# Kernel optimization log

Measured on AMD Instinct MI355X. Metric: run time of the kernel, lower is better.

The kernel has to match this reference:

```python
import jax, jax.numpy as jnp
import numpy as np

EMBED_DIM = 1024
NUM_HEADS = 16
HEAD_DIM = EMBED_DIM // NUM_HEADS  # 64


def setup_inputs() -> dict:
    key = jax.random.key(0)
    ks = jax.random.split(key, 9)
    B, S, E, D = 4, 2048, EMBED_DIM, HEAD_DIM
    s_e = 1.0 / np.sqrt(E)
    return {
        "x": jax.random.normal(ks[0], (B, S, E), dtype=jnp.float32),
        "Wq": jax.random.uniform(ks[1], (E, E), jnp.float32, -s_e, s_e),
        "bq": jax.random.uniform(ks[2], (E,), jnp.float32, -s_e, s_e),
        "Wk": jax.random.uniform(ks[3], (E, D), jnp.float32, -s_e, s_e),
        "bk": jax.random.uniform(ks[4], (D,), jnp.float32, -s_e, s_e),
        "Wv": jax.random.uniform(ks[5], (E, D), jnp.float32, -s_e, s_e),
        "bv": jax.random.uniform(ks[6], (D,), jnp.float32, -s_e, s_e),
        "Wo": jax.random.uniform(ks[7], (E, E), jnp.float32, -s_e, s_e),
        "bo": jax.random.uniform(ks[8], (E,), jnp.float32, -s_e, s_e),
    }


def reference(x, Wq, bq, Wk, bk, Wv, bv, Wo, bo):
    B, S, E = x.shape
    H, D = NUM_HEADS, HEAD_DIM
    q = (x @ Wq + bq).reshape(B, S, H, D)           # [B,S,H,D]
    k = x @ Wk + bk                                  # [B,S,D] shared single K head
    v = x @ Wv + bv                                  # [B,S,D] shared single V head
    scale = 1.0 / jnp.sqrt(jnp.asarray(D, x.dtype))
    # broadcast shared K across query heads: [B,H,Sq,Sk]
    scores = jnp.einsum("bqhd,bkd->bhqk", q, k) * scale
    probs = jax.nn.softmax(scores, axis=-1)
    out = jnp.einsum("bhqk,bkd->bqhd", probs, v).reshape(B, S, E)
    return out @ Wo + bo
```

## Files before the change

kernel.cpp:

```cpp
#include <hip/hip_runtime.h>

typedef short  bf16x8 __attribute__((ext_vector_type(8)));
typedef float  f32x4  __attribute__((ext_vector_type(4)));
typedef float  f32x16 __attribute__((ext_vector_type(16)));
typedef unsigned int u32;

__device__ __forceinline__ ushort f2b(float f) {
    union { float f; unsigned u; } c; c.f = f;
    unsigned r = c.u + 0x7fffu + ((c.u >> 16) & 1u);
    return (ushort)(r >> 16);
}

__device__ __forceinline__ unsigned cvtpk(float lo, float hi) {
    unsigned r;
    asm("v_cvt_pk_bf16_f32 %0, %1, %2" : "=v"(r) : "v"(lo), "v"(hi));
    return r;
}

__device__ __forceinline__ float fexp2(float x) {
#if __has_builtin(__builtin_amdgcn_exp2f)
    return __builtin_amdgcn_exp2f(x);
#else
    float r; asm("v_exp_f32 %0, %1" : "=v"(r) : "v"(x)); return r;
#endif
}

__device__ __forceinline__ void gload_lds16(const void* g, void* l) {
    __builtin_amdgcn_global_load_lds(
        (const __attribute__((address_space(1))) u32*)g,
        (__attribute__((address_space(3))) u32*)l, 16, 0, 0);
}

__global__ __launch_bounds__(256) void cast_f32_bf16(const float* __restrict__ in,
                                                     ushort* __restrict__ out, int n) {
    for (int i = (blockIdx.x * blockDim.x + threadIdx.x) * 4; i < n;
         i += gridDim.x * blockDim.x * 4) {
        float4 v = *(const float4*)(in + i);
        ushort4 o;
        o.x = f2b(v.x); o.y = f2b(v.y); o.z = f2b(v.z); o.w = f2b(v.w);
        *(ushort4*)(out + i) = o;
    }
}

__global__ __launch_bounds__(256) void transpose_cast(const float* __restrict__ in,
                                                      ushort* __restrict__ out, int R, int C) {
    __shared__ float tile[32][33];
    int c0 = blockIdx.x * 32, r0 = blockIdx.y * 32;
    int tx = threadIdx.x, ty = threadIdx.y;
#pragma unroll
    for (int i = 0; i < 32; i += 8)
        tile[ty + i][tx] = in[(size_t)(r0 + ty + i) * C + c0 + tx];
    __syncthreads();
#pragma unroll
    for (int i = 0; i < 32; i += 8)
        out[(size_t)(c0 + ty + i) * R + r0 + tx] = f2b(tile[tx][ty + i]);
}

__global__ void concat_bias(const float* __restrict__ bk, const float* __restrict__ bv,
                            float* __restrict__ o) {
    int i = threadIdx.x;
    if (i < 128) o[i] = (i < 64) ? bk[i] : bv[i - 64];
}

__global__ __launch_bounds__(256) void repack_kv(const ushort* __restrict__ kvb,
                                                 ushort* __restrict__ Kc,
                                                 ushort* __restrict__ Vc) {
    __shared__ ushort vl[64][72];
    int t = blockIdx.x, b = blockIdx.y;
    int tid = threadIdx.x;
#pragma unroll
    for (int u = tid; u < 512; u += 256) {
        int s = u >> 3, c = u & 7;
        const ushort* src = kvb + (size_t)(b * 2048 + t * 64 + s) * 128 + c * 8;
        *(uint4*)(Kc + ((size_t)(b * 8 + c) * 2048 + t * 64 + s) * 8) = *(const uint4*)src;
        *(uint4*)(&vl[s][c * 8]) = *(const uint4*)(src + 64);
    }
    __syncthreads();
#pragma unroll
    for (int u = tid; u < 512; u += 256) {
        int sc = u >> 6, d = u & 63;
        ushort tmp[8];
#pragma unroll
        for (int si = 0; si < 8; si++) tmp[si] = vl[sc * 8 + si][d];
        *(uint4*)(Vc + ((size_t)((b * 32 + t) * 8 + sc) * 64 + d) * 8) = *(uint4*)tmp;
    }
}

template <bool OUT_BF16>
__global__ __launch_bounds__(256) void gemm_bt(const ushort* __restrict__ A,
                                               const ushort* __restrict__ BT,
                                               const float* __restrict__ bias,
                                               void* __restrict__ Y, int M, int N, int K,
                                               float scale) {
    __shared__ ushort As[128 * 64];
    __shared__ ushort Bs[128 * 64];

    int nwg = gridDim.x * gridDim.y;
    int bid = blockIdx.y * gridDim.x + blockIdx.x;
    int swz = (bid & 7) * (nwg >> 3) + (bid >> 3);
    int bx = swz % gridDim.x, by = swz / gridDim.x;

    int m0 = by * 128, n0 = bx * 128;
    int t = threadIdx.x;
    int lane = t & 63, wid = t >> 6;
    int wr = wid >> 1, wc = wid & 1;
    int fr = lane & 15, fg = lane >> 4;

    int srow = wid * 32 + (lane >> 3);
    int scol = (lane & 7) * 8;
    const ushort* asrc = A + (size_t)(m0 + srow) * K + scol;
    const ushort* bsrc = BT + (size_t)(n0 + srow) * K + scol;

    f32x4 acc[4][4] = {};

    for (int kb = 0; kb < K; kb += 64) {
#pragma unroll
        for (int op = 0; op < 4; op++) {
            gload_lds16(asrc + kb + (size_t)op * 8 * K, &As[(wid * 32 + op * 8) * 64]);
            gload_lds16(bsrc + kb + (size_t)op * 8 * K, &Bs[(wid * 32 + op * 8) * 64]);
        }
        __syncthreads();
#pragma unroll
        for (int kk = 0; kk < 2; kk++) {
            bf16x8 af[4], bfr[4];
#pragma unroll
            for (int m = 0; m < 4; m++)
                af[m] = *(const bf16x8*)&As[(wr * 64 + m * 16 + fr) * 64 + kk * 32 + fg * 8];
#pragma unroll
            for (int n = 0; n < 4; n++)
                bfr[n] = *(const bf16x8*)&Bs[(wc * 64 + n * 16 + fr) * 64 + kk * 32 + fg * 8];
#pragma unroll
            for (int m = 0; m < 4; m++)
#pragma unroll
                for (int n = 0; n < 4; n++)
                    acc[m][n] = __builtin_amdgcn_mfma_f32_16x16x32_bf16(
                        af[m], bfr[n], acc[m][n], 0, 0, 0);
        }
        __syncthreads();
    }

#pragma unroll
    for (int m = 0; m < 4; m++)
#pragma unroll
        for (int n = 0; n < 4; n++) {
            int col = n0 + wc * 64 + n * 16 + fr;
            float bv = bias[col];
#pragma unroll
            for (int j = 0; j < 4; j++) {
                int row = m0 + wr * 64 + m * 16 + fg * 4 + j;
                float v = (acc[m][n][j] + bv) * scale;
                if (OUT_BF16)
                    ((ushort*)Y)[(size_t)row * N + col] = f2b(v);
                else
                    ((float*)Y)[(size_t)row * N + col] = v;
            }
        }
}

__global__ __launch_bounds__(256, 4) void attn_kernel(const ushort* __restrict__ qb,
                                                      const ushort* __restrict__ Kc,
                                                      const ushort* __restrict__ Vc,
                                                      ushort* __restrict__ ctx) {
    const int S = 2048, E = 1024;
    __shared__ ushort Kb[2][4096];
    __shared__ ushort Vb[2][4096];

    int b = blockIdx.z, h = blockIdx.y;
    int wid = threadIdx.x >> 6, lane = threadIdx.x & 63;
    int q0 = blockIdx.x * 128 + wid * 32;
    int ql = lane & 31, hi = lane >> 5;

    int c0 = wid * 2, c1 = c0 + 1;
    const ushort* ks0 = Kc + (size_t)(b * 8 + c0) * 2048 * 8 + lane * 8;
    const ushort* ks1 = Kc + (size_t)(b * 8 + c1) * 2048 * 8 + lane * 8;
    const ushort* vs0 = Vc + (size_t)(b * 32 * 8 + c0) * 64 * 8 + lane * 8;
    const ushort* vs1 = Vc + (size_t)(b * 32 * 8 + c1) * 64 * 8 + lane * 8;

    const ushort* qbase = qb + (size_t)(b * S + q0 + ql) * E + h * 64 + hi * 8;
    bf16x8 qf0 = *(const bf16x8*)(qbase);
    bf16x8 qf1 = *(const bf16x8*)(qbase + 16);
    bf16x8 qf2 = *(const bf16x8*)(qbase + 32);
    bf16x8 qf3 = *(const bf16x8*)(qbase + 48);

    const ushort* kb0 = &Kb[0][hi * 512 + ql * 8];
    const ushort* vb0 = &Vb[0][hi * 512 + ql * 8];

    f32x16 acc0 = {}, acc1 = {};
    f32x16 lv = {};

    gload_lds16(ks0, &Kb[0][c0 * 512]);
    gload_lds16(ks1, &Kb[0][c1 * 512]);
    gload_lds16(vs0, &Vb[0][c0 * 512]);
    gload_lds16(vs1, &Vb[0][c1 * 512]);
    __syncthreads();

    int cur = 0;
    for (int t = 0; t < 32; ++t) {
        if (t < 31) {
            int nb = cur ^ 1;
            ks0 += 512; ks1 += 512; vs0 += 4096; vs1 += 4096;
            gload_lds16(ks0, &Kb[nb][c0 * 512]);
            gload_lds16(ks1, &Kb[nb][c1 * 512]);
            gload_lds16(vs0, &Vb[nb][c0 * 512]);
            gload_lds16(vs1, &Vb[nb][c1 * 512]);
        }
        const ushort* kp = kb0 + cur * 4096;
        const ushort* vp = vb0 + cur * 4096;

        f32x16 pt0 = {}, pt1 = {};
#pragma unroll
        for (int s = 0; s < 4; s++) {
            bf16x8 kf0 = *(const bf16x8*)(kp + s * 1024);
            bf16x8 kf1 = *(const bf16x8*)(kp + s * 1024 + 256);
            bf16x8 qs = (s == 0) ? qf0 : (s == 1) ? qf1 : (s == 2) ? qf2 : qf3;
            pt0 = __builtin_amdgcn_mfma_f32_32x32x16_bf16(kf0, qs, pt0, 0, 0, 0);
            pt1 = __builtin_amdgcn_mfma_f32_32x32x16_bf16(kf1, qs, pt1, 0, 0, 0);
        }

#pragma unroll
        for (int r = 0; r < 16; r++) pt0[r] = fexp2(pt0[r]);
#pragma unroll
        for (int r = 0; r < 16; r++) pt1[r] = fexp2(pt1[r]);

#pragma unroll
        for (int ks = 0; ks < 4; ks++) {
            float p0, p1, p2, p3, p4, p5, p6, p7;
            if (ks == 0)      { p0=pt0[0]; p1=pt0[1]; p2=pt0[2]; p3=pt0[3];
                                p4=pt0[4]; p5=pt0[5]; p6=pt0[6]; p7=pt0[7]; }
            else if (ks == 1) { p0=pt0[8]; p1=pt0[9]; p2=pt0[10]; p3=pt0[11];
                                p4=pt0[12]; p5=pt0[13]; p6=pt0[14]; p7=pt0[15]; }
            else if (ks == 2) { p0=pt1[0]; p1=pt1[1]; p2=pt1[2]; p3=pt1[3];
                                p4=pt1[4]; p5=pt1[5]; p6=pt1[6]; p7=pt1[7]; }
            else              { p0=pt1[8]; p1=pt1[9]; p2=pt1[10]; p3=pt1[11];
                                p4=pt1[12]; p5=pt1[13]; p6=pt1[14]; p7=pt1[15]; }
            unsigned w0 = cvtpk(p0, p1);
            unsigned w2 = cvtpk(p4, p5);
            asm volatile("v_permlane32_swap_b32 %0, %1" : "+v"(w0), "+v"(w2));
            unsigned w1 = cvtpk(p2, p3);
            unsigned w3 = cvtpk(p6, p7);
            asm volatile("v_permlane32_swap_b32 %0, %1" : "+v"(w1), "+v"(w3));
            bf16x8 pa;
            ((unsigned*)&pa)[0] = w0;
            ((unsigned*)&pa)[1] = w1;
            ((unsigned*)&pa)[2] = w2;
            ((unsigned*)&pa)[3] = w3;

            bf16x8 va0 = *(const bf16x8*)(vp + ks * 1024);
            bf16x8 va1 = *(const bf16x8*)(vp + ks * 1024 + 256);
            acc0 = __builtin_amdgcn_mfma_f32_32x32x16_bf16(va0, pa, acc0, 0, 0, 0);
            acc1 = __builtin_amdgcn_mfma_f32_32x32x16_bf16(va1, pa, acc1, 0, 0, 0);
        }

        lv = lv + pt0;
        lv = lv + pt1;

        __syncthreads();
        cur ^= 1;
    }

    float v[16];
#pragma unroll
    for (int r = 0; r < 16; r++) v[r] = lv[r];
#pragma unroll
    for (int st = 8; st; st >>= 1)
#pragma unroll
        for (int r = 0; r < 8; r++)
            if (r < st) v[r] = v[r] + v[r + st];
    float l = v[0] + __shfl_xor(v[0], 32);
    float inv = 1.f / l;

    ushort* obase = ctx + (size_t)(b * S + q0 + ql) * E + h * 64;
#pragma unroll
    for (int g = 0; g < 4; g++) {
        int d = 8 * g + 4 * hi;
        ushort4 o;
        o.x = f2b(acc0[4 * g + 0] * inv);
        o.y = f2b(acc0[4 * g + 1] * inv);
        o.z = f2b(acc0[4 * g + 2] * inv);
        o.w = f2b(acc0[4 * g + 3] * inv);
        *(ushort4*)(obase + d) = o;
    }
#pragma unroll
    for (int g = 0; g < 4; g++) {
        int d = 32 + 8 * g + 4 * hi;
        ushort4 o;
        o.x = f2b(acc1[4 * g + 0] * inv);
        o.y = f2b(acc1[4 * g + 1] * inv);
        o.z = f2b(acc1[4 * g + 2] * inv);
        o.w = f2b(acc1[4 * g + 3] * inv);
        *(ushort4*)(obase + d) = o;
    }
}

extern "C" void kernel_launch(void* const* d_in, const int* in_sizes, int n_in,
                              void* d_out, int out_size, void* d_ws, size_t ws_size,
                              hipStream_t stream) {
    const int B = 4, S = 2048, E = 1024, D = 64;
    const int M = B * S;
    const float QSCALE = 0.18033688011112042f;

    const float* x  = (const float*)d_in[0];
    const float* Wq = (const float*)d_in[1];
    const float* bq = (const float*)d_in[2];
    const float* Wk = (const float*)d_in[3];
    const float* bk = (const float*)d_in[4];
    const float* Wv = (const float*)d_in[5];
    const float* bv = (const float*)d_in[6];
    const float* Wo = (const float*)d_in[7];
    const float* bo = (const float*)d_in[8];
    float* out = (float*)d_out;

    char* w = (char*)d_ws;
    ushort* xb   = (ushort*)w;                 w += (size_t)M * E * 2;
    ushort* qb   = (ushort*)w;                 w += (size_t)M * E * 2;
    ushort* ctx  = (ushort*)w;                 w += (size_t)M * E * 2;
    ushort* WqT  = (ushort*)w;                 w += (size_t)E * E * 2;
    ushort* WoT  = (ushort*)w;                 w += (size_t)E * E * 2;
    ushort* WkvT = (ushort*)w;                 w += (size_t)128 * E * 2;
    ushort* kvb  = (ushort*)w;                 w += (size_t)M * 128 * 2;
    ushort* Kc   = (ushort*)w;                 w += (size_t)B * 8 * S * 8 * 2;
    ushort* Vc   = (ushort*)w;                 w += (size_t)B * 32 * 8 * 64 * 8 * 2;
    float*  bkv  = (float*)w;                  w += 512;

    cast_f32_bf16<<<2048, 256, 0, stream>>>(x, xb, M * E);
    transpose_cast<<<dim3(32, 32), dim3(32, 8), 0, stream>>>(Wq, WqT, E, E);
    transpose_cast<<<dim3(2, 32),  dim3(32, 8), 0, stream>>>(Wk, WkvT, E, D);
    transpose_cast<<<dim3(2, 32),  dim3(32, 8), 0, stream>>>(Wv, WkvT + (size_t)64 * E, E, D);
    transpose_cast<<<dim3(32, 32), dim3(32, 8), 0, stream>>>(Wo, WoT, E, E);
    concat_bias<<<1, 128, 0, stream>>>(bk, bv, bkv);

    gemm_bt<true><<<dim3(E / 128, M / 128), 256, 0, stream>>>(xb, WqT, bq, qb, M, E, E, QSCALE);
    gemm_bt<true><<<dim3(1, M / 128), 256, 0, stream>>>(xb, WkvT, bkv, kvb, M, 128, E, 1.0f);
    repack_kv<<<dim3(32, 4), 256, 0, stream>>>(kvb, Kc, Vc);

    attn_kernel<<<dim3(S / 128, 16, B), 256, 0, stream>>>(qb, Kc, Vc, ctx);

    gemm_bt<false><<<dim3(E / 128, M / 128), 256, 0, stream>>>(ctx, WoT, bo, (void*)out, M, E, E, 1.0f);
}
```

Before: 183.1 us.

## Fuse Q and KV projections into one QKV GEMM and batch transposes

```diff
diff --git a/kernel.cpp b/kernel.cpp
--- a/kernel.cpp
+++ b/kernel.cpp
@@ -42,9 +42,14 @@
     }
 }
 
-__global__ __launch_bounds__(256) void transpose_cast(const float* __restrict__ in,
-                                                      ushort* __restrict__ out, int R, int C) {
+__global__ __launch_bounds__(256) void transpose_cast2(const float* __restrict__ in0,
+                                                       ushort* __restrict__ out0,
+                                                       const float* __restrict__ in1,
+                                                       ushort* __restrict__ out1,
+                                                       int R, int C) {
     __shared__ float tile[32][33];
+    const float* in = blockIdx.z ? in1 : in0;
+    ushort* out = blockIdx.z ? out1 : out0;
     int c0 = blockIdx.x * 32, r0 = blockIdx.y * 32;
     int tx = threadIdx.x, ty = threadIdx.y;
 #pragma unroll
@@ -56,13 +61,13 @@
         out[(size_t)(c0 + ty + i) * R + r0 + tx] = f2b(tile[tx][ty + i]);
 }
 
-__global__ void concat_bias(const float* __restrict__ bk, const float* __restrict__ bv,
-                            float* __restrict__ o) {
-    int i = threadIdx.x;
-    if (i < 128) o[i] = (i < 64) ? bk[i] : bv[i - 64];
-}
-
-__global__ __launch_bounds__(256) void repack_kv(const ushort* __restrict__ kvb,
+__global__ void concat_bias3(const float* __restrict__ bq, const float* __restrict__ bk,
+                             const float* __restrict__ bv, float* __restrict__ o) {
+    for (int i = threadIdx.x; i < 1152; i += 256)
+        o[i] = (i < 1024) ? bq[i] : (i < 1088) ? bk[i - 1024] : bv[i - 1088];
+}
+
+__global__ __launch_bounds__(256) void repack_kv(const ushort* __restrict__ qkv,
                                                  ushort* __restrict__ Kc,
                                                  ushort* __restrict__ Vc) {
     __shared__ ushort vl[64][72];
@@ -71,7 +76,7 @@
 #pragma unroll
     for (int u = tid; u < 512; u += 256) {
         int s = u >> 3, c = u & 7;
-        const ushort* src = kvb + (size_t)(b * 2048 + t * 64 + s) * 128 + c * 8;
+        const ushort* src = qkv + (size_t)(b * 2048 + t * 64 + s) * 1152 + 1024 + c * 8;
         *(uint4*)(Kc + ((size_t)(b * 8 + c) * 2048 + t * 64 + s) * 8) = *(const uint4*)src;
         *(uint4*)(&vl[s][c * 8]) = *(const uint4*)(src + 64);
     }
@@ -91,7 +96,7 @@
                                                const ushort* __restrict__ BT,
                                                const float* __restrict__ bias,
                                                void* __restrict__ Y, int M, int N, int K,
-                                               float scale) {
+                                               int nq, float scale) {
     __shared__ ushort As[128 * 64];
     __shared__ ushort Bs[128 * 64];
 
@@ -145,10 +150,11 @@
         for (int n = 0; n < 4; n++) {
             int col = n0 + wc * 64 + n * 16 + fr;
             float bv = bias[col];
+            float sc = (col < nq) ? scale : 1.0f;
 #pragma unroll
             for (int j = 0; j < 4; j++) {
                 int row = m0 + wr * 64 + m * 16 + fg * 4 + j;
-                float v = (acc[m][n][j] + bv) * scale;
+                float v = (acc[m][n][j] + bv) * sc;
                 if (OUT_BF16)
                     ((ushort*)Y)[(size_t)row * N + col] = f2b(v);
                 else
@@ -157,11 +163,11 @@
         }
 }
 
-__global__ __launch_bounds__(256, 4) void attn_kernel(const ushort* __restrict__ qb,
+__global__ __launch_bounds__(256, 4) void attn_kernel(const ushort* __restrict__ qkv,
                                                       const ushort* __restrict__ Kc,
                                                       const ushort* __restrict__ Vc,
                                                       ushort* __restrict__ ctx) {
-    const int S = 2048, E = 1024;
+    const int S = 2048, E = 1024, QSTR = 1152;
     __shared__ ushort Kb[2][4096];
     __shared__ ushort Vb[2][4096];
 
@@ -176,7 +182,7 @@
     const ushort* vs0 = Vc + (size_t)(b * 32 * 8 + c0) * 64 * 8 + lane * 8;
     const ushort* vs1 = Vc + (size_t)(b * 32 * 8 + c1) * 64 * 8 + lane * 8;
 
-    const ushort* qbase = qb + (size_t)(b * S + q0 + ql) * E + h * 64 + hi * 8;
+    const ushort* qbase = qkv + (size_t)(b * S + q0 + ql) * QSTR + h * 64 + hi * 8;
     bf16x8 qf0 = *(const bf16x8*)(qbase);
     bf16x8 qf1 = *(const bf16x8*)(qbase + 16);
     bf16x8 qf2 = *(const bf16x8*)(qbase + 32);
@@ -208,6 +214,7 @@
         const ushort* vp = vb0 + cur * 4096;
 
         f32x16 pt0 = {}, pt1 = {};
+        __builtin_amdgcn_s_setprio(1);
 #pragma unroll
         for (int s = 0; s < 4; s++) {
             bf16x8 kf0 = *(const bf16x8*)(kp + s * 1024);
@@ -216,12 +223,14 @@
             pt0 = __builtin_amdgcn_mfma_f32_32x32x16_bf16(kf0, qs, pt0, 0, 0, 0);
             pt1 = __builtin_amdgcn_mfma_f32_32x32x16_bf16(kf1, qs, pt1, 0, 0, 0);
         }
+        __builtin_amdgcn_s_setprio(0);
 
 #pragma unroll
         for (int r = 0; r < 16; r++) pt0[r] = fexp2(pt0[r]);
 #pragma unroll
         for (int r = 0; r < 16; r++) pt1[r] = fexp2(pt1[r]);
 
+        __builtin_amdgcn_s_setprio(1);
 #pragma unroll
         for (int ks = 0; ks < 4; ks++) {
             float p0, p1, p2, p3, p4, p5, p6, p7;
@@ -250,6 +259,7 @@
             acc0 = __builtin_amdgcn_mfma_f32_32x32x16_bf16(va0, pa, acc0, 0, 0, 0);
             acc1 = __builtin_amdgcn_mfma_f32_32x32x16_bf16(va1, pa, acc1, 0, 0, 0);
         }
+        __builtin_amdgcn_s_setprio(0);
 
         lv = lv + pt0;
         lv = lv + pt1;
@@ -297,6 +307,7 @@
                               hipStream_t stream) {
     const int B = 4, S = 2048, E = 1024, D = 64;
     const int M = B * S;
+    const int NQKV = 1152;
     const float QSCALE = 0.18033688011112042f;
 
     const float* x  = (const float*)d_in[0];
@@ -311,29 +322,28 @@
     float* out = (float*)d_out;
 
     char* w = (char*)d_ws;
-    ushort* xb   = (ushort*)w;                 w += (size_t)M * E * 2;
-    ushort* qb   = (ushort*)w;                 w += (size_t)M * E * 2;
-    ushort* ctx  = (ushort*)w;                 w += (size_t)M * E * 2;
-    ushort* WqT  = (ushort*)w;                 w += (size_t)E * E * 2;
-    ushort* WoT  = (ushort*)w;                 w += (size_t)E * E * 2;
-    ushort* WkvT = (ushort*)w;                 w += (size_t)128 * E * 2;
-    ushort* kvb  = (ushort*)w;                 w += (size_t)M * 128 * 2;
-    ushort* Kc   = (ushort*)w;                 w += (size_t)B * 8 * S * 8 * 2;
-    ushort* Vc   = (ushort*)w;                 w += (size_t)B * 32 * 8 * 64 * 8 * 2;
-    float*  bkv  = (float*)w;                  w += 512;
+    ushort* xb    = (ushort*)w;                w += (size_t)M * E * 2;
+    ushort* qkv   = (ushort*)w;                w += (size_t)M * NQKV * 2;
+    ushort* ctx   = (ushort*)w;                w += (size_t)M * E * 2;
+    ushort* WqkvT = (ushort*)w;                w += (size_t)NQKV * E * 2;
+    ushort* WoT   = (ushort*)w;                w += (size_t)E * E * 2;
+    ushort* Kc    = (ushort*)w;                w += (size_t)B * 8 * S * 8 * 2;
+    ushort* Vc    = (ushort*)w;                w += (size_t)B * 32 * 8 * 64 * 8 * 2;
+    float*  bqkv  = (float*)w;                 w += 8192;
 
     cast_f32_bf16<<<2048, 256, 0, stream>>>(x, xb, M * E);
-    transpose_cast<<<dim3(32, 32), dim3(32, 8), 0, stream>>>(Wq, WqT, E, E);
-    transpose_cast<<<dim3(2, 32),  dim3(32, 8), 0, stream>>>(Wk, WkvT, E, D);
-    transpose_cast<<<dim3(2, 32),  dim3(32, 8), 0, stream>>>(Wv, WkvT + (size_t)64 * E, E, D);
-    transpose_cast<<<dim3(32, 32), dim3(32, 8), 0, stream>>>(Wo, WoT, E, E);
-    concat_bias<<<1, 128, 0, stream>>>(bk, bv, bkv);
-
-    gemm_bt<true><<<dim3(E / 128, M / 128), 256, 0, stream>>>(xb, WqT, bq, qb, M, E, E, QSCALE);
-    gemm_bt<true><<<dim3(1, M / 128), 256, 0, stream>>>(xb, WkvT, bkv, kvb, M, 128, E, 1.0f);
-    repack_kv<<<dim3(32, 4), 256, 0, stream>>>(kvb, Kc, Vc);
-
-    attn_kernel<<<dim3(S / 128, 16, B), 256, 0, stream>>>(qb, Kc, Vc, ctx);
-
-    gemm_bt<false><<<dim3(E / 128, M / 128), 256, 0, stream>>>(ctx, WoT, bo, (void*)out, M, E, E, 1.0f);
-}
+    transpose_cast2<<<dim3(32, 32, 2), dim3(32, 8), 0, stream>>>(
+        Wq, WqkvT, Wo, WoT, E, E);
+    transpose_cast2<<<dim3(2, 32, 2), dim3(32, 8), 0, stream>>>(
+        Wk, WqkvT + (size_t)1024 * E, Wv, WqkvT + (size_t)1088 * E, E, D);
+    concat_bias3<<<1, 256, 0, stream>>>(bq, bk, bv, bqkv);
+
+    gemm_bt<true><<<dim3(NQKV / 128, M / 128), 256, 0, stream>>>(
+        xb, WqkvT, bqkv, qkv, M, NQKV, E, 1024, QSCALE);
+    repack_kv<<<dim3(32, 4), 256, 0, stream>>>(qkv, Kc, Vc);
+
+    attn_kernel<<<dim3(S / 128, 16, B), 256, 0, stream>>>(qkv, Kc, Vc, ctx);
+
+    gemm_bt<false><<<dim3(E / 128, M / 128), 256, 0, stream>>>(
+        ctx, WoT, bo, (void*)out, M, E, E, 0, 1.0f);
+}
```

After: 174.6 us. 1.05x faster.
